# Optimization experiments

Hardware: AMD Instinct MI355X
Metric: run time of the kernel (lower is better)

## Reference

```python
import jax, jax.numpy as jnp
import numpy as np

N, K, C, L = 8192, 12, 128, 6
FF = 4 * C
SIG_LO, SIG_HI = 1.0, 5.0
BOX = 25.0

TRI_NAMES = ("ln_g", "ln_b", "Wa", "ba", "Wga", "bga", "Wb", "bb", "Wgb", "bgb",
             "lno_g", "lno_b", "Wo", "bo", "Wgo", "bgo")
FFN_NAMES = ("ln_g", "ln_b", "W1", "b1", "W2", "b2")


def _ln(x, g, b, eps=1e-5):
    m = jnp.mean(x, axis=-1, keepdims=True)
    v = jnp.mean((x - m) ** 2, axis=-1, keepdims=True)
    return (x - m) * jax.lax.rsqrt(v + eps) * g + b


def _knn_embed(coords):
    # pairwise distances -> k smallest (self included), Gaussian RBF bank over C sigmas
    d2 = jnp.sum((coords[:, None, :] - coords[None, :, :]) ** 2, axis=-1)  # [N,N]
    dist = jnp.sqrt(jnp.maximum(d2, 0.0))
    neg_d, nbr = jax.lax.top_k(-dist, K)                      # [N,K]
    k_dist = -neg_d
    sig = jnp.linspace(SIG_LO, SIG_HI, C)                     # [C]
    g = jnp.exp(-(k_dist[..., None] ** 2) / (2.0 * sig ** 2))  # [N,K,C]
    vals = jnp.where(g > 0.1, g, 0.0)                         # threshold as in repo
    vals = jnp.where(jnp.isnan(vals), 0.0, vals)
    return nbr, vals


def _transpose_vals(v, nbr):
    # sparse rowcol_transpose: value of edge (j,i) aligned to slot of edge (i,j); 0 if absent
    n = nbr.shape[0]
    nn = nbr[nbr]                                   # [N,K,K]: neighbor lists of each neighbor j
    eq = nn == jnp.arange(n)[:, None, None]         # slot where j lists i back
    pos = jnp.argmax(eq, axis=-1)                   # [N,K]
    found = jnp.any(eq, axis=-1)                    # [N,K]
    tv = v[nbr, pos]                                # [N,K,C] value at edge (j,i)
    return jnp.where(found[..., None], tv, jnp.zeros_like(tv))


def _tri_update(v, nbr, p, incoming):
    x = _ln(v, p["ln_g"], p["ln_b"])
    a = jax.nn.sigmoid(x @ p["Wga"] + p["bga"]) * (x @ p["Wa"] + p["ba"])
    b = jax.nn.sigmoid(x @ p["Wgb"] + p["bgb"]) * (x @ p["Wb"] + p["bb"])
    if incoming:  # column/incoming update operates on transposed edges
        a = _transpose_vals(a, nbr)
        b = _transpose_vals(b, nbr)
    # sparse triangle multiplicative update over KNN neighbor slots
    k = jnp.einsum('ntc,nmtc->nmc', a, b[nbr])      # [N,K,C]
    o = _ln(k, p["lno_g"], p["lno_b"]) @ p["Wo"] + p["bo"]
    return jax.nn.sigmoid(x @ p["Wgo"] + p["bgo"]) * o


def _ffn(v, p):
    x = _ln(v, p["ln_g"], p["ln_b"])
    return jax.nn.gelu(x @ p["W1"] + p["b1"], approximate=False) @ p["W2"] + p["b2"]


def _forward(coords, tri, ffn, dec_W, dec_b):
    nbr, v = _knn_embed(coords)
    v = jax.lax.stop_gradient(v)  # embedding runs under torch.no_grad in the original

    def step(v, lp):
        tp, fp = lp
        p_row = {n: t[0] for n, t in zip(TRI_NAMES, tp)}
        p_col = {n: t[1] for n, t in zip(TRI_NAMES, tp)}
        v = v + _tri_update(v, nbr, p_row, False)   # row (outgoing) update
        v = v + _tri_update(v, nbr, p_col, True)    # col (incoming) update
        v = v + _ffn(v, dict(zip(FFN_NAMES, fp)))
        return v, None

    v, _ = jax.lax.scan(jax.checkpoint(step), v, (tri, ffn))
    s = v + _transpose_vals(v, nbr)                 # sparse_operation(edge, edge^T, op='sum')
    e = s @ dec_W + dec_b                           # [N,K,1] decode
    rows = jnp.repeat(jnp.arange(N), K)
    dense = jnp.zeros((N, N, e.shape[-1]), e.dtype)
    dense = dense.at[rows, nbr.reshape(-1)].add(e.reshape(-1, e.shape[-1]))
    return dense                                    # [N,N,1] like .to_dense()


def setup_inputs() -> dict:
    key = jax.random.key(0)
    ks = jax.random.split(key, 8)
    coords = jax.random.uniform(ks[0], (N, 3), jnp.float32) * BOX

    def lin(k, fin, fout, pre=()):
        kw, _ = jax.random.split(k)
        W = jax.random.normal(kw, pre + (fin, fout), jnp.float32) / np.sqrt(fin).astype(np.float32)
        b = jnp.zeros(pre + (fout,), jnp.float32)
        return W, b

    inp = {"coords": coords}
    k_iter = iter(jax.random.split(ks[1], 16))
    pre = (L, 2)
    inp["tri_ln_g"] = jnp.ones(pre + (C,), jnp.float32)
    inp["tri_ln_b"] = jnp.zeros(pre + (C,), jnp.float32)
    for nm in ("a", "ga", "b", "gb", "o", "go"):
        W, b = lin(next(k_iter), C, C, pre)
        inp[f"tri_W{nm}"] = W
        inp[f"tri_b{nm}"] = b
    inp["tri_lno_g"] = jnp.ones(pre + (C,), jnp.float32)
    inp["tri_lno_b"] = jnp.zeros(pre + (C,), jnp.float32)
    inp["ffn_ln_g"] = jnp.ones((L, C), jnp.float32)
    inp["ffn_ln_b"] = jnp.zeros((L, C), jnp.float32)
    inp["ffn_W1"], inp["ffn_b1"] = lin(next(k_iter), C, FF, (L,))
    inp["ffn_W2"], inp["ffn_b2"] = lin(next(k_iter), FF, C, (L,))
    inp["dec_W"], inp["dec_b"] = lin(next(k_iter), C, 1)
    return inp


def reference(coords, tri_ln_g, tri_ln_b, tri_Wa, tri_ba, tri_Wga, tri_bga,
              tri_Wb, tri_bb, tri_Wgb, tri_bgb, tri_lno_g, tri_lno_b,
              tri_Wo, tri_bo, tri_Wgo, tri_bgo,
              ffn_ln_g, ffn_ln_b, ffn_W1, ffn_b1, ffn_W2, ffn_b2,
              dec_W, dec_b):
    tri = (tri_ln_g, tri_ln_b, tri_Wa, tri_ba, tri_Wga, tri_bga,
           tri_Wb, tri_bb, tri_Wgb, tri_bgb, tri_lno_g, tri_lno_b,
           tri_Wo, tri_bo, tri_Wgo, tri_bgo)
    ffn = (ffn_ln_g, ffn_ln_b, ffn_W1, ffn_b1, ffn_W2, ffn_b2)
    return _forward(coords, tri, ffn, dec_W, dec_b)
```

## Files before the change

### kernel.cpp

```cpp
#include <hip/hip_runtime.h>
#include <hip/hip_bf16.h>
#include <stdint.h>
#include <stddef.h>

#define NPTS 8192
#define KNN  12
#define CH   128
#define FFD  512
#define MEDGE (NPTS * KNN)

typedef __attribute__((ext_vector_type(8))) _Float16 half8;
typedef __attribute__((ext_vector_type(4))) _Float16 half4;
typedef __attribute__((ext_vector_type(4))) float f32x4;

__device__ __forceinline__ float wave_sum(float v) {
#pragma unroll
  for (int off = 32; off > 0; off >>= 1) v += __shfl_xor(v, off, 64);
  return v;
}
__device__ __forceinline__ float sigm_(float x) { return 1.0f / (1.0f + expf(-x)); }
__device__ __forceinline__ float gelu_(float x) { return 0.5f * x * (1.0f + erff(x * 0.7071067811865475f)); }

__global__ __launch_bounds__(256)
void prep_coords(const float* __restrict__ c, float4* __restrict__ c4)
{
  int i = blockIdx.x * 256 + threadIdx.x;
  if (i < NPTS) c4[i] = make_float4(c[3 * i], c[3 * i + 1], c[3 * i + 2], 0.0f);
}

struct SwzArgs {
  const float* src[8];
  _Float16* dst[8];
  int K[8], N[8], B[8], perB[8];
};

__global__ __launch_bounds__(256)
void prep_weights_swz(SwzArgs sa)
{
  int g = blockIdx.y;
  int idx = blockIdx.x * 256 + threadIdx.x;
  int perB = sa.perB[g];
  if (idx >= sa.B[g] * perB) return;
  int K = sa.K[g], N = sa.N[g];
  int b = idx / perB;
  int c = idx - b * perB;
  int l16 = c & 15;
  int quad = (c >> 4) & 3;
  int rest = c >> 6;
  int kts = K >> 5;
  int kt = rest % kts;
  int mt = rest / kts;
  const float* sp = sa.src[g] + ((size_t)b * K + kt * 32 + quad * 8) * N + mt * 16 + l16;
  _Float16* dp = sa.dst[g] + ((size_t)b * perB + c) * 8;
#pragma unroll
  for (int e = 0; e < 8; ++e) dp[e] = (_Float16)sp[(size_t)e * N];
}

#define KNN_CAP 2048

__global__ __launch_bounds__(256)
void knn_embed(const float4* __restrict__ coords4, const float* __restrict__ lng,
               const float* __restrict__ lnb, int* __restrict__ nbr,
               float* __restrict__ v0, _Float16* __restrict__ xln)
{
#pragma clang fp contract(off)
  __shared__ unsigned long long buf[KNN_CAP];
  __shared__ unsigned long long sel[KNN];
  __shared__ int cnt_s;
  const int i = blockIdx.x;
  const int tid = threadIdx.x;
  const int lane = tid & 63;
  const int wv = tid >> 6;
  const float4 ci = coords4[i];

  float T2 = 9.0f;
  int cnt;
  while (true) {
    if (tid == 0) cnt_s = 0;
    __syncthreads();
    for (int j = tid; j < NPTS; j += 256) {
      float4 cj = coords4[j];
      float dx = ci.x - cj.x;
      float dy = ci.y - cj.y;
      float dz = ci.z - cj.z;
      float d2 = dx * dx + dy * dy + dz * dz;
      if (d2 < T2) {
        unsigned long long key =
            (((unsigned long long)__float_as_uint(sqrtf(d2))) << 32) | (unsigned int)j;
        int idx = atomicAdd(&cnt_s, 1);
        if (idx < KNN_CAP) buf[idx] = key;
      }
    }
    __syncthreads();
    cnt = cnt_s;
    if (cnt >= KNN) break;
    T2 *= 4.0f;
    __syncthreads();
  }
  if (cnt > KNN_CAP) cnt = KNN_CAP;

  if (wv == 0) {
    unsigned long long best[KNN];
#pragma unroll
    for (int q = 0; q < KNN; ++q) best[q] = ~0ULL;
    for (int p2 = lane; p2 < cnt; p2 += 64) {
      unsigned long long key = buf[p2];
      if (key < best[KNN - 1]) {
        best[KNN - 1] = key;
#pragma unroll
        for (int q = KNN - 2; q >= 0; --q) {
          if (best[q + 1] < best[q]) { unsigned long long t = best[q]; best[q] = best[q + 1]; best[q + 1] = t; }
        }
      }
    }
    int p = 0;
    for (int r = 0; r < KNN; ++r) {
      unsigned long long c = ~0ULL;
#pragma unroll
      for (int q = 0; q < KNN; ++q) if (q == p) c = best[q];
      unsigned long long m = c;
#pragma unroll
      for (int off = 32; off > 0; off >>= 1) {
        unsigned long long o = __shfl_xor(m, off, 64);
        if (o < m) m = o;
      }
      if (c == m) ++p;
      if (lane == 0) sel[r] = m;
    }
  }
  __syncthreads();
  if (tid < KNN) nbr[i * KNN + tid] = (int)(unsigned int)(sel[tid] & 0xFFFFFFFFULL);

  float g1 = lng[lane], g2 = lng[lane + 64];
  float bb1 = lnb[lane], bb2 = lnb[lane + 64];
  for (int k = wv * 3; k < wv * 3 + 3; ++k) {
    float d = __uint_as_float((unsigned int)(sel[k] >> 32));
    float sig1 = (float)(1.0 + 4.0 * (double)lane / 127.0);
    float sig2 = (float)(1.0 + 4.0 * (double)(lane + 64) / 127.0);
    float e1 = expf((-(d * d)) / (2.0f * sig1 * sig1));
    float e2 = expf((-(d * d)) / (2.0f * sig2 * sig2));
    float v1 = (e1 > 0.1f) ? e1 : 0.0f;
    float v2 = (e2 > 0.1f) ? e2 : 0.0f;
    size_t off = (size_t)(i * KNN + k) * CH;
    v0[off + lane] = v1;
    v0[off + lane + 64] = v2;
    float m = wave_sum(v1 + v2) * (1.0f / 128.0f);
    float d1 = v1 - m, d2 = v2 - m;
    float var = wave_sum(d1 * d1 + d2 * d2) * (1.0f / 128.0f);
    float rs = 1.0f / sqrtf(var + 1e-5f);
    xln[off + lane]      = (_Float16)(d1 * rs * g1 + bb1);
    xln[off + lane + 64] = (_Float16)(d2 * rs * g2 + bb2);
  }
}

__global__ __launch_bounds__(256)
void build_tidx(const int* __restrict__ nbr, int* __restrict__ tidx)
{
  int e = blockIdx.x * 256 + threadIdx.x;
  if (e >= MEDGE) return;
  int i = e / KNN;
  int j = nbr[e];
  int res = -1;
#pragma unroll
  for (int t = 0; t < KNN; ++t) {
    if (nbr[j * KNN + t] == i) { res = j * KNN + t; break; }
  }
  tidx[e] = res;
}

__global__ __launch_bounds__(256)
void gemm_ab_go(const _Float16* __restrict__ xln,
                const _Float16* __restrict__ wa,  const float* __restrict__ ba,
                const _Float16* __restrict__ wga, const float* __restrict__ bga,
                const _Float16* __restrict__ wb,  const float* __restrict__ bb,
                const _Float16* __restrict__ wgb, const float* __restrict__ bgb,
                const _Float16* __restrict__ wgo, const float* __restrict__ bgo,
                _Float16* __restrict__ aout, _Float16* __restrict__ bout,
                _Float16* __restrict__ gobout)
{
  const int lane = threadIdx.x & 63;
  const int quad = lane >> 4;
  const int l16 = lane & 15;
  const int gw = blockIdx.x * 4 + (threadIdx.x >> 6);
  const int base = gw * 32;
  const int chbase = quad * 16 + l16;

  half8 xf[2][4];
#pragma unroll
  for (int rt = 0; rt < 2; ++rt)
#pragma unroll
    for (int kt = 0; kt < 4; ++kt)
      xf[rt][kt] = *(const half8*)(xln + (size_t)(base + rt * 16 + l16) * CH + kt * 32 + quad * 8);

  const half8* WA  = (const half8*)wa;
  const half8* WGA = (const half8*)wga;
  const half8* WB  = (const half8*)wb;
  const half8* WGB = (const half8*)wgb;
  const half8* WGO = (const half8*)wgo;

#pragma unroll
  for (int mt = 0; mt < 8; ++mt) {
    f32x4 aA[2], aGA[2], aB[2], aGB[2], aGO[2];
    const f32x4 z = {0.f, 0.f, 0.f, 0.f};
#pragma unroll
    for (int rt = 0; rt < 2; ++rt) { aA[rt] = z; aGA[rt] = z; aB[rt] = z; aGB[rt] = z; aGO[rt] = z; }
#pragma unroll
    for (int kt = 0; kt < 4; ++kt) {
      int ch = (mt * 4 + kt) * 64 + chbase;
      half8 wfa = WA[ch], wfga = WGA[ch], wfb = WB[ch], wfgb = WGB[ch], wfgo = WGO[ch];
#pragma unroll
      for (int rt = 0; rt < 2; ++rt) {
        aA[rt]  = __builtin_amdgcn_mfma_f32_16x16x32_f16(wfa,  xf[rt][kt], aA[rt], 0, 0, 0);
        aGA[rt] = __builtin_amdgcn_mfma_f32_16x16x32_f16(wfga, xf[rt][kt], aGA[rt], 0, 0, 0);
        aB[rt]  = __builtin_amdgcn_mfma_f32_16x16x32_f16(wfb,  xf[rt][kt], aB[rt], 0, 0, 0);
        aGB[rt] = __builtin_amdgcn_mfma_f32_16x16x32_f16(wfgb, xf[rt][kt], aGB[rt], 0, 0, 0);
        aGO[rt] = __builtin_amdgcn_mfma_f32_16x16x32_f16(wfgo, xf[rt][kt], aGO[rt], 0, 0, 0);
      }
    }
    f32x4 bva  = *(const f32x4*)(ba  + mt * 16 + quad * 4);
    f32x4 bvga = *(const f32x4*)(bga + mt * 16 + quad * 4);
    f32x4 bvb  = *(const f32x4*)(bb  + mt * 16 + quad * 4);
    f32x4 bvgb = *(const f32x4*)(bgb + mt * 16 + quad * 4);
    f32x4 bvgo = *(const f32x4*)(bgo + mt * 16 + quad * 4);
#pragma unroll
    for (int rt = 0; rt < 2; ++rt) {
      half4 av, bv, gv;
#pragma unroll
      for (int r = 0; r < 4; ++r) {
        av[r] = (_Float16)(sigm_(aGA[rt][r] + bvga[r]) * (aA[rt][r] + bva[r]));
        bv[r] = (_Float16)(sigm_(aGB[rt][r] + bvgb[r]) * (aB[rt][r] + bvb[r]));
        gv[r] = (_Float16)(sigm_(aGO[rt][r] + bvgo[r]));
      }
      size_t off = (size_t)(base + rt * 16 + l16) * CH + mt * 16 + quad * 4;
      *(half4*)(aout + off) = av;
      *(half4*)(bout + off) = bv;
      *(half4*)(gobout + off) = gv;
    }
  }
}

__global__ __launch_bounds__(192)
void tri_og(const _Float16* __restrict__ a, const _Float16* __restrict__ b,
            const int* __restrict__ nbr, const int* __restrict__ tidx,
            const float* __restrict__ lng, const float* __restrict__ lnb,
            const _Float16* __restrict__ wo, const float* __restrict__ bo,
            const _Float16* __restrict__ gob, float* __restrict__ v,
            const float* __restrict__ nlng, const float* __restrict__ nlnb,
            _Float16* __restrict__ xlnN, int incoming)
{
  __shared__ alignas(16) _Float16 As[48][136];
  __shared__ alignas(16) _Float16 klds[48][136];
  __shared__ int bidx[4][KNN][KNN];
  __shared__ int nbr_s[4][KNN];
  const int n0 = blockIdx.x * 4;
  const int tid = threadIdx.x;

  if (tid < 48) nbr_s[tid / KNN][tid % KNN] = nbr[n0 * KNN + tid];
  __syncthreads();
  for (int it = tid; it < 4 * KNN * KNN; it += 192) {
    int nn = it / (KNN * KNN);
    int r = it - nn * KNN * KNN;
    int m = r / KNN, t = r - m * KNN;
    int j = nbr_s[nn][m];
    bidx[nn][m][t] = incoming ? tidx[j * KNN + t] : (j * KNN + t);
  }
  for (int it = tid; it < 4 * KNN * 16; it += 192) {
    int nn = it / (KNN * 16);
    int r = it - nn * (KNN * 16);
    int t = r >> 4;
    int c8 = (r & 15) * 8;
    half8 av;
    if (incoming) {
      int ti = tidx[(size_t)(n0 + nn) * KNN + t];
      if (ti >= 0) av = *(const half8*)(a + (size_t)ti * CH + c8);
      else {
#pragma unroll
        for (int e = 0; e < 8; ++e) av[e] = (_Float16)0.0f;
      }
    } else {
      av = *(const half8*)(a + (size_t)((n0 + nn) * KNN + t) * CH + c8);
    }
    *(half8*)&As[nn * KNN + t][c8] = av;
  }
  __syncthreads();

  const int m2 = tid >> 4;
  const int c8 = (tid & 15) * 8;
  for (int nn = 0; nn < 4; ++nn) {
    float acc[8];
#pragma unroll
    for (int r = 0; r < 8; ++r) acc[r] = 0.0f;
#pragma unroll
    for (int t = 0; t < KNN; ++t) {
      int bi = bidx[nn][m2][t];
      if (bi >= 0) {
        half8 bv = *(const half8*)(b + (size_t)bi * CH + c8);
        half8 av = *(const half8*)&As[nn * KNN + t][c8];
#pragma unroll
        for (int r = 0; r < 8; ++r) acc[r] += (float)av[r] * (float)bv[r];
      }
    }
    float s = 0.0f, sq = 0.0f;
#pragma unroll
    for (int r = 0; r < 8; ++r) { s += acc[r]; sq += acc[r] * acc[r]; }
#pragma unroll
    for (int off = 1; off < 16; off <<= 1) {
      s += __shfl_xor(s, off, 64);
      sq += __shfl_xor(sq, off, 64);
    }
    float mean = s * (1.0f / 128.0f);
    float var = sq * (1.0f / 128.0f) - mean * mean;
    if (var < 0.0f) var = 0.0f;
    float rs = 1.0f / sqrtf(var + 1e-5f);
    half8 o;
#pragma unroll
    for (int r = 0; r < 8; ++r)
      o[r] = (_Float16)((acc[r] - mean) * rs * lng[c8 + r] + lnb[c8 + r]);
    *(half8*)&klds[nn * KNN + m2][c8] = o;
  }
  __syncthreads();

  const int lane = tid & 63;
  const int w = tid >> 6;
  const int quad = lane >> 4;
  const int l16 = lane & 15;
  const int chbase = quad * 16 + l16;
  const size_t rowOff = (size_t)(blockIdx.x * 48 + w * 16 + l16) * CH;

  half8 kf[4];
#pragma unroll
  for (int kt = 0; kt < 4; ++kt)
    kf[kt] = *(const half8*)&klds[w * 16 + l16][kt * 32 + quad * 8];

  const half8* WO = (const half8*)wo;
  f32x4 vn[8];
  float s = 0.0f, sq = 0.0f;
#pragma unroll
  for (int mt = 0; mt < 8; ++mt) {
    f32x4 acc = {0.f, 0.f, 0.f, 0.f};
#pragma unroll
    for (int kt = 0; kt < 4; ++kt)
      acc = __builtin_amdgcn_mfma_f32_16x16x32_f16(WO[(mt * 4 + kt) * 64 + chbase], kf[kt], acc, 0, 0, 0);
    half4 g4 = *(const half4*)(gob + rowOff + mt * 16 + quad * 4);
    f32x4 bo4 = *(const f32x4*)(bo + mt * 16 + quad * 4);
    f32x4 vv = *(const f32x4*)(v + rowOff + mt * 16 + quad * 4);
#pragma unroll
    for (int r = 0; r < 4; ++r) {
      float nv = vv[r] + (float)g4[r] * (acc[r] + bo4[r]);
      vn[mt][r] = nv;
      s += nv;
      sq += nv * nv;
    }
    *(f32x4*)(v + rowOff + mt * 16 + quad * 4) = vn[mt];
  }
  s  += __shfl_xor(s, 16, 64);  s  += __shfl_xor(s, 32, 64);
  sq += __shfl_xor(sq, 16, 64); sq += __shfl_xor(sq, 32, 64);
  float mean = s * (1.0f / 128.0f);
  float var = sq * (1.0f / 128.0f) - mean * mean;
  if (var < 0.0f) var = 0.0f;
  float rs = 1.0f / sqrtf(var + 1e-5f);
#pragma unroll
  for (int mt = 0; mt < 8; ++mt) {
    f32x4 g4 = *(const f32x4*)(nlng + mt * 16 + quad * 4);
    f32x4 b4 = *(const f32x4*)(nlnb + mt * 16 + quad * 4);
    half4 o;
#pragma unroll
    for (int r = 0; r < 4; ++r)
      o[r] = (_Float16)((vn[mt][r] - mean) * rs * g4[r] + b4[r]);
    *(half4*)(xlnN + rowOff + mt * 16 + quad * 4) = o;
  }
}

#define HADDR(row, ch) ((((row) * 64 + ((ch) ^ ((row) & 7)))) * 8)

__global__ __launch_bounds__(256)
void ffn_fused(const _Float16* __restrict__ xln,
               const _Float16* __restrict__ w1, const float* __restrict__ b1,
               const _Float16* __restrict__ w2, const float* __restrict__ b2,
               float* __restrict__ v,
               const float* __restrict__ nlng, const float* __restrict__ nlnb,
               _Float16* __restrict__ xlnN)
{
  __shared__ alignas(16) _Float16 hlds[32 * FFD];
  __shared__ float part[32][4][2];
  const int tid = threadIdx.x;
  const int lane = tid & 63;
  const int w = tid >> 6;
  const int quad = lane >> 4;
  const int l16 = lane & 15;
  const int rowBase = blockIdx.x * 32;
  const int chbase = quad * 16 + l16;

  half8 xf[2][4];
#pragma unroll
  for (int rt = 0; rt < 2; ++rt)
#pragma unroll
    for (int kt = 0; kt < 4; ++kt)
      xf[rt][kt] = *(const half8*)(xln + (size_t)(rowBase + rt * 16 + l16) * CH + kt * 32 + quad * 8);

  const half8* W1 = (const half8*)w1;
#pragma unroll
  for (int mt = 0; mt < 8; ++mt) {
    int mtg = w * 8 + mt;
    f32x4 acc[2];
    const f32x4 z = {0.f, 0.f, 0.f, 0.f};
    acc[0] = z; acc[1] = z;
#pragma unroll
    for (int kt = 0; kt < 4; ++kt) {
      half8 wf = W1[(mtg * 4 + kt) * 64 + chbase];
#pragma unroll
      for (int rt = 0; rt < 2; ++rt)
        acc[rt] = __builtin_amdgcn_mfma_f32_16x16x32_f16(wf, xf[rt][kt], acc[rt], 0, 0, 0);
    }
    f32x4 bv = *(const f32x4*)(b1 + mtg * 16 + quad * 4);
    int ch = mtg * 2 + (quad >> 1);
    int sub = (quad & 1) * 4;
#pragma unroll
    for (int rt = 0; rt < 2; ++rt) {
      int row = rt * 16 + l16;
      half4 hh;
#pragma unroll
      for (int r = 0; r < 4; ++r)
        hh[r] = (_Float16)(gelu_(acc[rt][r] + bv[r]));
      *(half4*)&hlds[HADDR(row, ch) + sub] = hh;
    }
  }
  __syncthreads();

  const half8* W2 = (const half8*)w2;
  f32x4 vn2[2][2];
  float s2[2] = {0.f, 0.f}, q2[2] = {0.f, 0.f};
#pragma unroll
  for (int m2 = 0; m2 < 2; ++m2) {
    int mt = w * 2 + m2;
    f32x4 accA[2], accB[2];
    const f32x4 z = {0.f, 0.f, 0.f, 0.f};
    accA[0] = z; accA[1] = z; accB[0] = z; accB[1] = z;
#pragma unroll
    for (int kt = 0; kt < 16; kt += 2) {
      half8 wf0 = W2[(mt * 16 + kt) * 64 + chbase];
      half8 wf1 = W2[(mt * 16 + kt + 1) * 64 + chbase];
#pragma unroll
      for (int rt = 0; rt < 2; ++rt) {
        int row = rt * 16 + l16;
        half8 hf0 = *(const half8*)&hlds[HADDR(row, kt * 4 + quad)];
        half8 hf1 = *(const half8*)&hlds[HADDR(row, (kt + 1) * 4 + quad)];
        accA[rt] = __builtin_amdgcn_mfma_f32_16x16x32_f16(wf0, hf0, accA[rt], 0, 0, 0);
        accB[rt] = __builtin_amdgcn_mfma_f32_16x16x32_f16(wf1, hf1, accB[rt], 0, 0, 0);
      }
    }
    f32x4 bv = *(const f32x4*)(b2 + mt * 16 + quad * 4);
#pragma unroll
    for (int rt = 0; rt < 2; ++rt) {
      size_t off = (size_t)(rowBase + rt * 16 + l16) * CH + mt * 16 + quad * 4;
      f32x4 vv = *(const f32x4*)(v + off);
#pragma unroll
      for (int r = 0; r < 4; ++r) {
        float nv = vv[r] + accA[rt][r] + accB[rt][r] + bv[r];
        vn2[m2][rt][r] = nv;
        s2[rt] += nv;
        q2[rt] += nv * nv;
      }
      *(f32x4*)(v + off) = vn2[m2][rt];
    }
  }
#pragma unroll
  for (int rt = 0; rt < 2; ++rt) {
    float ss = s2[rt], qq = q2[rt];
    ss += __shfl_xor(ss, 16, 64); ss += __shfl_xor(ss, 32, 64);
    qq += __shfl_xor(qq, 16, 64); qq += __shfl_xor(qq, 32, 64);
    if (quad == 0) { part[rt * 16 + l16][w][0] = ss; part[rt * 16 + l16][w][1] = qq; }
  }
  __syncthreads();
#pragma unroll
  for (int rt = 0; rt < 2; ++rt) {
    int row = rt * 16 + l16;
    float su = part[row][0][0] + part[row][1][0] + part[row][2][0] + part[row][3][0];
    float qu = part[row][0][1] + part[row][1][1] + part[row][2][1] + part[row][3][1];
    float mean = su * (1.0f / 128.0f);
    float var = qu * (1.0f / 128.0f) - mean * mean;
    if (var < 0.0f) var = 0.0f;
    float rs = 1.0f / sqrtf(var + 1e-5f);
#pragma unroll
    for (int m2 = 0; m2 < 2; ++m2) {
      int mt = w * 2 + m2;
      f32x4 g4 = *(const f32x4*)(nlng + mt * 16 + quad * 4);
      f32x4 b4 = *(const f32x4*)(nlnb + mt * 16 + quad * 4);
      half4 o;
#pragma unroll
      for (int r = 0; r < 4; ++r)
        o[r] = (_Float16)((vn2[m2][rt][r] - mean) * rs * g4[r] + b4[r]);
      *(half4*)(xlnN + (size_t)(rowBase + row) * CH + mt * 16 + quad * 4) = o;
    }
  }
}

__global__ __launch_bounds__(256)
void decode_row(const float* __restrict__ vin, const int* __restrict__ tidx,
                const int* __restrict__ nbr, const float* __restrict__ decW,
                const float* __restrict__ decB, float* __restrict__ out)
{
  __shared__ float ev[KNN];
  __shared__ int nbr_s[KNN];
  const int n = blockIdx.x;
  const int tid = threadIdx.x;
  const int lane = tid & 63;
  const int w = tid >> 6;
  if (tid < KNN) nbr_s[tid] = nbr[n * KNN + tid];
  float dw1 = decW[lane], dw2 = decW[lane + 64];
  for (int k = w; k < KNN; k += 4) {
    int e = n * KNN + k;
    int ti = tidx[e];
    float s1 = vin[(size_t)e * CH + lane];
    float s2 = vin[(size_t)e * CH + 64 + lane];
    if (ti >= 0) {
      s1 += vin[(size_t)ti * CH + lane];
      s2 += vin[(size_t)ti * CH + 64 + lane];
    }
    float tot = wave_sum(s1 * dw1 + s2 * dw2);
    if (lane == 0) ev[k] = tot + decB[0];
  }
  __syncthreads();
  float4 z = make_float4(0.f, 0.f, 0.f, 0.f);
  float4* row = (float4*)(out + (size_t)n * NPTS);
  for (int idx = tid; idx < NPTS / 4; idx += 256) row[idx] = z;
  __syncthreads();
  if (tid < KNN) out[(size_t)n * NPTS + nbr_s[tid]] = ev[tid];
}

extern "C" void kernel_launch(void* const* d_in, const int* in_sizes, int n_in,
                              void* d_out, int out_size, void* d_ws, size_t ws_size,
                              hipStream_t stream)
{
  (void)in_sizes; (void)n_in; (void)out_size; (void)ws_size;
  const float* coords  = (const float*)d_in[0];
  const float* t_ln_g  = (const float*)d_in[1];
  const float* t_ln_b  = (const float*)d_in[2];
  const float* t_Wa    = (const float*)d_in[3];
  const float* t_ba    = (const float*)d_in[4];
  const float* t_Wga   = (const float*)d_in[5];
  const float* t_bga   = (const float*)d_in[6];
  const float* t_Wb    = (const float*)d_in[7];
  const float* t_bb    = (const float*)d_in[8];
  const float* t_Wgb   = (const float*)d_in[9];
  const float* t_bgb   = (const float*)d_in[10];
  const float* t_Wo    = (const float*)d_in[11];
  const float* t_bo    = (const float*)d_in[12];
  const float* t_Wgo   = (const float*)d_in[13];
  const float* t_bgo   = (const float*)d_in[14];
  const float* t_lno_g = (const float*)d_in[15];
  const float* t_lno_b = (const float*)d_in[16];
  const float* f_ln_g  = (const float*)d_in[17];
  const float* f_ln_b  = (const float*)d_in[18];
  const float* f_W1    = (const float*)d_in[19];
  const float* f_b1    = (const float*)d_in[20];
  const float* f_W2    = (const float*)d_in[21];
  const float* f_b2    = (const float*)d_in[22];
  const float* dec_W   = (const float*)d_in[23];
  const float* dec_b   = (const float*)d_in[24];

  const size_t NKC = (size_t)MEDGE * CH;
  char* ws = (char*)d_ws;
  float* v        = (float*)(ws);
  _Float16* gx    = (_Float16*)(ws + NKC * 6);
  int* nbr        = (int*)(ws + NKC * 8);
  int* tidx       = (int*)(ws + NKC * 8 + (size_t)MEDGE * 4);
  float4* coords4 = (float4*)(ws + NKC * 8 + (size_t)MEDGE * 8);
  _Float16* wbase = (_Float16*)(ws + NKC * 8 + (size_t)MEDGE * 8 + NPTS * 16);
  const size_t TRIH = (size_t)12 * 2048 * 8;
  _Float16* wA  = wbase;
  _Float16* wGA = wA  + TRIH;
  _Float16* wB  = wGA + TRIH;
  _Float16* wGB = wB  + TRIH;
  _Float16* wGO = wGB + TRIH;
  _Float16* wO  = wGO + TRIH;
  _Float16* w1  = wO  + TRIH;
  _Float16* w2  = w1  + (size_t)6 * 8192 * 8;

  _Float16* abuf = (_Float16*)d_out;
  _Float16* bbuf = abuf + NKC;

  prep_coords<<<32, 256, 0, stream>>>(coords, coords4);

  SwzArgs sa;
  sa.src[0] = t_Wa;  sa.dst[0] = wA;  sa.K[0] = CH;  sa.N[0] = CH;  sa.B[0] = 12; sa.perB[0] = 2048;
  sa.src[1] = t_Wga; sa.dst[1] = wGA; sa.K[1] = CH;  sa.N[1] = CH;  sa.B[1] = 12; sa.perB[1] = 2048;
  sa.src[2] = t_Wb;  sa.dst[2] = wB;  sa.K[2] = CH;  sa.N[2] = CH;  sa.B[2] = 12; sa.perB[2] = 2048;
  sa.src[3] = t_Wgb; sa.dst[3] = wGB; sa.K[3] = CH;  sa.N[3] = CH;  sa.B[3] = 12; sa.perB[3] = 2048;
  sa.src[4] = t_Wgo; sa.dst[4] = wGO; sa.K[4] = CH;  sa.N[4] = CH;  sa.B[4] = 12; sa.perB[4] = 2048;
  sa.src[5] = t_Wo;  sa.dst[5] = wO;  sa.K[5] = CH;  sa.N[5] = CH;  sa.B[5] = 12; sa.perB[5] = 2048;
  sa.src[6] = f_W1;  sa.dst[6] = w1;  sa.K[6] = CH;  sa.N[6] = FFD; sa.B[6] = 6;  sa.perB[6] = 8192;
  sa.src[7] = f_W2;  sa.dst[7] = w2;  sa.K[7] = FFD; sa.N[7] = CH;  sa.B[7] = 6;  sa.perB[7] = 8192;
  dim3 pgrid(192, 8);
  prep_weights_swz<<<pgrid, 256, 0, stream>>>(sa);

  knn_embed<<<NPTS, 256, 0, stream>>>(coords4, t_ln_g, t_ln_b, nbr, v, gx);
  build_tidx<<<MEDGE / 256, 256, 0, stream>>>(nbr, tidx);

  const size_t WS = (size_t)2048 * 8;
  gemm_ab_go<<<MEDGE / 128, 256, 0, stream>>>(gx,
      wA, t_ba, wGA, t_bga, wB, t_bb, wGB, t_bgb, wGO, t_bgo,
      abuf, bbuf, gx);

  for (int l = 0; l < 6; ++l) {
    int s0 = 2 * l, s1 = 2 * l + 1, s2 = 2 * l + 2;
    tri_og<<<NPTS / 4, 192, 0, stream>>>(abuf, bbuf, nbr, tidx,
        t_lno_g + s0 * CH, t_lno_b + s0 * CH,
        wO + s0 * WS, t_bo + s0 * CH, gx, v,
        t_ln_g + s1 * CH, t_ln_b + s1 * CH, gx, 0);
    gemm_ab_go<<<MEDGE / 128, 256, 0, stream>>>(gx,
        wA + s1 * WS, t_ba + s1 * CH, wGA + s1 * WS, t_bga + s1 * CH,
        wB + s1 * WS, t_bb + s1 * CH, wGB + s1 * WS, t_bgb + s1 * CH,
        wGO + s1 * WS, t_bgo + s1 * CH,
        abuf, bbuf, gx);
    tri_og<<<NPTS / 4, 192, 0, stream>>>(abuf, bbuf, nbr, tidx,
        t_lno_g + s1 * CH, t_lno_b + s1 * CH,
        wO + s1 * WS, t_bo + s1 * CH, gx, v,
        f_ln_g + l * CH, f_ln_b + l * CH, gx, 1);
    const float* ng = (l < 5) ? (t_ln_g + s2 * CH) : t_ln_g;
    const float* nb = (l < 5) ? (t_ln_b + s2 * CH) : t_ln_b;
    ffn_fused<<<MEDGE / 32, 256, 0, stream>>>(gx,
        w1 + (size_t)l * 8192 * 8, f_b1 + l * FFD,
        w2 + (size_t)l * 8192 * 8, f_b2 + l * CH,
        v, ng, nb, gx);
    if (l < 5) {
      gemm_ab_go<<<MEDGE / 128, 256, 0, stream>>>(gx,
          wA + s2 * WS, t_ba + s2 * CH, wGA + s2 * WS, t_bga + s2 * CH,
          wB + s2 * WS, t_bb + s2 * CH, wGB + s2 * WS, t_bgb + s2 * CH,
          wGO + s2 * WS, t_bgo + s2 * CH,
          abuf, bbuf, gx);
    }
  }

  decode_row<<<NPTS, 256, 0, stream>>>(v, tidx, nbr, dec_W, dec_b, (float*)d_out);
}
```

Measured before the change: 2.563 ms.

## Fuse next-stage gated projection GEMMs into triangle and FFN epilogues

```diff
diff --git a/kernel.cpp b/kernel.cpp
--- a/kernel.cpp
+++ b/kernel.cpp
@@ -20,6 +20,8 @@
 }
 __device__ __forceinline__ float sigm_(float x) { return 1.0f / (1.0f + expf(-x)); }
 __device__ __forceinline__ float gelu_(float x) { return 0.5f * x * (1.0f + erff(x * 0.7071067811865475f)); }
+
+#define XADDR(row, ch) ((((row) * 16 + ((ch) ^ ((row) & 7)))) * 8)
 
 __global__ __launch_bounds__(256)
 void prep_coords(const float* __restrict__ c, float4* __restrict__ c4)
@@ -240,13 +242,19 @@
 }
 
 __global__ __launch_bounds__(192)
-void tri_og(const _Float16* __restrict__ a, const _Float16* __restrict__ b,
-            const int* __restrict__ nbr, const int* __restrict__ tidx,
-            const float* __restrict__ lng, const float* __restrict__ lnb,
-            const _Float16* __restrict__ wo, const float* __restrict__ bo,
-            const _Float16* __restrict__ gob, float* __restrict__ v,
-            const float* __restrict__ nlng, const float* __restrict__ nlnb,
-            _Float16* __restrict__ xlnN, int incoming)
+void tri_og_ab(const _Float16* __restrict__ a, const _Float16* __restrict__ b,
+               const int* __restrict__ nbr, const int* __restrict__ tidx,
+               const float* __restrict__ lng, const float* __restrict__ lnb,
+               const _Float16* __restrict__ wo, const float* __restrict__ bo,
+               const _Float16* __restrict__ gob, float* __restrict__ v,
+               const float* __restrict__ nlng, const float* __restrict__ nlnb,
+               const _Float16* __restrict__ wa,  const float* __restrict__ ba,
+               const _Float16* __restrict__ wga, const float* __restrict__ bga,
+               const _Float16* __restrict__ wb,  const float* __restrict__ bb,
+               const _Float16* __restrict__ wgb, const float* __restrict__ bgb,
+               const _Float16* __restrict__ wgo2, const float* __restrict__ bgo2,
+               _Float16* __restrict__ aout, _Float16* __restrict__ bout,
+               _Float16* __restrict__ gobout, int incoming)
 {
   __shared__ alignas(16) _Float16 As[48][136];
   __shared__ alignas(16) _Float16 klds[48][136];
@@ -325,12 +333,14 @@
   const int quad = lane >> 4;
   const int l16 = lane & 15;
   const int chbase = quad * 16 + l16;
-  const size_t rowOff = (size_t)(blockIdx.x * 48 + w * 16 + l16) * CH;
+  const int rowL = w * 16 + l16;
+  const size_t rowOff = (size_t)(blockIdx.x * 48 + rowL) * CH;
+  _Float16* xsw = &As[0][0];
 
   half8 kf[4];
 #pragma unroll
   for (int kt = 0; kt < 4; ++kt)
-    kf[kt] = *(const half8*)&klds[w * 16 + l16][kt * 32 + quad * 8];
+    kf[kt] = *(const half8*)&klds[rowL][kt * 32 + quad * 8];
 
   const half8* WO = (const half8*)wo;
   f32x4 vn[8];
@@ -367,6 +377,178 @@
 #pragma unroll
     for (int r = 0; r < 4; ++r)
       o[r] = (_Float16)((vn[mt][r] - mean) * rs * g4[r] + b4[r]);
+    int ch = mt * 2 + (quad >> 1);
+    *(half4*)&xsw[XADDR(rowL, ch) + (quad & 1) * 4] = o;
+  }
+  half8 xf[4];
+#pragma unroll
+  for (int kt = 0; kt < 4; ++kt)
+    xf[kt] = *(const half8*)&xsw[XADDR(rowL, kt * 4 + quad)];
+
+  const half8* WA  = (const half8*)wa;
+  const half8* WGA = (const half8*)wga;
+  const half8* WB  = (const half8*)wb;
+  const half8* WGB = (const half8*)wgb;
+  const half8* WGO = (const half8*)wgo2;
+#pragma unroll
+  for (int mt = 0; mt < 8; ++mt) {
+    f32x4 aA = {0.f,0.f,0.f,0.f}, aGA = aA, aB = aA, aGB = aA, aGO = aA;
+#pragma unroll
+    for (int kt = 0; kt < 4; ++kt) {
+      int ch = (mt * 4 + kt) * 64 + chbase;
+      aA  = __builtin_amdgcn_mfma_f32_16x16x32_f16(WA[ch],  xf[kt], aA, 0, 0, 0);
+      aGA = __builtin_amdgcn_mfma_f32_16x16x32_f16(WGA[ch], xf[kt], aGA, 0, 0, 0);
+      aB  = __builtin_amdgcn_mfma_f32_16x16x32_f16(WB[ch],  xf[kt], aB, 0, 0, 0);
+      aGB = __builtin_amdgcn_mfma_f32_16x16x32_f16(WGB[ch], xf[kt], aGB, 0, 0, 0);
+      aGO = __builtin_amdgcn_mfma_f32_16x16x32_f16(WGO[ch], xf[kt], aGO, 0, 0, 0);
+    }
+    f32x4 bva  = *(const f32x4*)(ba   + mt * 16 + quad * 4);
+    f32x4 bvga = *(const f32x4*)(bga  + mt * 16 + quad * 4);
+    f32x4 bvb  = *(const f32x4*)(bb   + mt * 16 + quad * 4);
+    f32x4 bvgb = *(const f32x4*)(bgb  + mt * 16 + quad * 4);
+    f32x4 bvgo = *(const f32x4*)(bgo2 + mt * 16 + quad * 4);
+    half4 av, bv, gv;
+#pragma unroll
+    for (int r = 0; r < 4; ++r) {
+      av[r] = (_Float16)(sigm_(aGA[r] + bvga[r]) * (aA[r] + bva[r]));
+      bv[r] = (_Float16)(sigm_(aGB[r] + bvgb[r]) * (aB[r] + bvb[r]));
+      gv[r] = (_Float16)(sigm_(aGO[r] + bvgo[r]));
+    }
+    size_t off = rowOff + mt * 16 + quad * 4;
+    *(half4*)(aout + off) = av;
+    *(half4*)(bout + off) = bv;
+    *(half4*)(gobout + off) = gv;
+  }
+}
+
+__global__ __launch_bounds__(192)
+void tri_og(const _Float16* __restrict__ a, const _Float16* __restrict__ b,
+            const int* __restrict__ nbr, const int* __restrict__ tidx,
+            const float* __restrict__ lng, const float* __restrict__ lnb,
+            const _Float16* __restrict__ wo, const float* __restrict__ bo,
+            const _Float16* __restrict__ gob, float* __restrict__ v,
+            const float* __restrict__ nlng, const float* __restrict__ nlnb,
+            _Float16* __restrict__ xlnN, int incoming)
+{
+  __shared__ alignas(16) _Float16 As[48][136];
+  __shared__ alignas(16) _Float16 klds[48][136];
+  __shared__ int bidx[4][KNN][KNN];
+  __shared__ int nbr_s[4][KNN];
+  const int n0 = blockIdx.x * 4;
+  const int tid = threadIdx.x;
+
+  if (tid < 48) nbr_s[tid / KNN][tid % KNN] = nbr[n0 * KNN + tid];
+  __syncthreads();
+  for (int it = tid; it < 4 * KNN * KNN; it += 192) {
+    int nn = it / (KNN * KNN);
+    int r = it - nn * KNN * KNN;
+    int m = r / KNN, t = r - m * KNN;
+    int j = nbr_s[nn][m];
+    bidx[nn][m][t] = incoming ? tidx[j * KNN + t] : (j * KNN + t);
+  }
+  for (int it = tid; it < 4 * KNN * 16; it += 192) {
+    int nn = it / (KNN * 16);
+    int r = it - nn * (KNN * 16);
+    int t = r >> 4;
+    int c8 = (r & 15) * 8;
+    half8 av;
+    if (incoming) {
+      int ti = tidx[(size_t)(n0 + nn) * KNN + t];
+      if (ti >= 0) av = *(const half8*)(a + (size_t)ti * CH + c8);
+      else {
+#pragma unroll
+        for (int e = 0; e < 8; ++e) av[e] = (_Float16)0.0f;
+      }
+    } else {
+      av = *(const half8*)(a + (size_t)((n0 + nn) * KNN + t) * CH + c8);
+    }
+    *(half8*)&As[nn * KNN + t][c8] = av;
+  }
+  __syncthreads();
+
+  const int m2 = tid >> 4;
+  const int c8 = (tid & 15) * 8;
+  for (int nn = 0; nn < 4; ++nn) {
+    float acc[8];
+#pragma unroll
+    for (int r = 0; r < 8; ++r) acc[r] = 0.0f;
+#pragma unroll
+    for (int t = 0; t < KNN; ++t) {
+      int bi = bidx[nn][m2][t];
+      if (bi >= 0) {
+        half8 bv = *(const half8*)(b + (size_t)bi * CH + c8);
+        half8 av = *(const half8*)&As[nn * KNN + t][c8];
+#pragma unroll
+        for (int r = 0; r < 8; ++r) acc[r] += (float)av[r] * (float)bv[r];
+      }
+    }
+    float s = 0.0f, sq = 0.0f;
+#pragma unroll
+    for (int r = 0; r < 8; ++r) { s += acc[r]; sq += acc[r] * acc[r]; }
+#pragma unroll
+    for (int off = 1; off < 16; off <<= 1) {
+      s += __shfl_xor(s, off, 64);
+      sq += __shfl_xor(sq, off, 64);
+    }
+    float mean = s * (1.0f / 128.0f);
+    float var = sq * (1.0f / 128.0f) - mean * mean;
+    if (var < 0.0f) var = 0.0f;
+    float rs = 1.0f / sqrtf(var + 1e-5f);
+    half8 o;
+#pragma unroll
+    for (int r = 0; r < 8; ++r)
+      o[r] = (_Float16)((acc[r] - mean) * rs * lng[c8 + r] + lnb[c8 + r]);
+    *(half8*)&klds[nn * KNN + m2][c8] = o;
+  }
+  __syncthreads();
+
+  const int lane = tid & 63;
+  const int w = tid >> 6;
+  const int quad = lane >> 4;
+  const int l16 = lane & 15;
+  const int chbase = quad * 16 + l16;
+  const size_t rowOff = (size_t)(blockIdx.x * 48 + w * 16 + l16) * CH;
+
+  half8 kf[4];
+#pragma unroll
+  for (int kt = 0; kt < 4; ++kt)
+    kf[kt] = *(const half8*)&klds[w * 16 + l16][kt * 32 + quad * 8];
+
+  const half8* WO = (const half8*)wo;
+  f32x4 vn[8];
+  float s = 0.0f, sq = 0.0f;
+#pragma unroll
+  for (int mt = 0; mt < 8; ++mt) {
+    f32x4 acc = {0.f, 0.f, 0.f, 0.f};
+#pragma unroll
+    for (int kt = 0; kt < 4; ++kt)
+      acc = __builtin_amdgcn_mfma_f32_16x16x32_f16(WO[(mt * 4 + kt) * 64 + chbase], kf[kt], acc, 0, 0, 0);
+    half4 g4 = *(const half4*)(gob + rowOff + mt * 16 + quad * 4);
+    f32x4 bo4 = *(const f32x4*)(bo + mt * 16 + quad * 4);
+    f32x4 vv = *(const f32x4*)(v + rowOff + mt * 16 + quad * 4);
+#pragma unroll
+    for (int r = 0; r < 4; ++r) {
+      float nv = vv[r] + (float)g4[r] * (acc[r] + bo4[r]);
+      vn[mt][r] = nv;
+      s += nv;
+      sq += nv * nv;
+    }
+    *(f32x4*)(v + rowOff + mt * 16 + quad * 4) = vn[mt];
+  }
+  s  += __shfl_xor(s, 16, 64);  s  += __shfl_xor(s, 32, 64);
+  sq += __shfl_xor(sq, 16, 64); sq += __shfl_xor(sq, 32, 64);
+  float mean = s * (1.0f / 128.0f);
+  float var = sq * (1.0f / 128.0f) - mean * mean;
+  if (var < 0.0f) var = 0.0f;
+  float rs = 1.0f / sqrtf(var + 1e-5f);
+#pragma unroll
+  for (int mt = 0; mt < 8; ++mt) {
+    f32x4 g4 = *(const f32x4*)(nlng + mt * 16 + quad * 4);
+    f32x4 b4 = *(const f32x4*)(nlnb + mt * 16 + quad * 4);
+    half4 o;
+#pragma unroll
+    for (int r = 0; r < 4; ++r)
+      o[r] = (_Float16)((vn[mt][r] - mean) * rs * g4[r] + b4[r]);
     *(half4*)(xlnN + rowOff + mt * 16 + quad * 4) = o;
   }
 }
@@ -374,12 +556,18 @@
 #define HADDR(row, ch) ((((row) * 64 + ((ch) ^ ((row) & 7)))) * 8)
 
 __global__ __launch_bounds__(256)
-void ffn_fused(const _Float16* __restrict__ xln,
-               const _Float16* __restrict__ w1, const float* __restrict__ b1,
-               const _Float16* __restrict__ w2, const float* __restrict__ b2,
-               float* __restrict__ v,
-               const float* __restrict__ nlng, const float* __restrict__ nlnb,
-               _Float16* __restrict__ xlnN)
+void ffn_ab(const _Float16* __restrict__ xln,
+            const _Float16* __restrict__ w1, const float* __restrict__ b1,
+            const _Float16* __restrict__ w2, const float* __restrict__ b2,
+            float* __restrict__ v,
+            const float* __restrict__ nlng, const float* __restrict__ nlnb,
+            const _Float16* __restrict__ wa,  const float* __restrict__ ba,
+            const _Float16* __restrict__ wga, const float* __restrict__ bga,
+            const _Float16* __restrict__ wb,  const float* __restrict__ bb,
+            const _Float16* __restrict__ wgb, const float* __restrict__ bgb,
+            const _Float16* __restrict__ wgo2, const float* __restrict__ bgo2,
+            _Float16* __restrict__ aout, _Float16* __restrict__ bout,
+            _Float16* __restrict__ gobout, int doAB)
 {
   __shared__ alignas(16) _Float16 hlds[32 * FFD];
   __shared__ float part[32][4][2];
@@ -464,6 +652,8 @@
       *(f32x4*)(v + off) = vn2[m2][rt];
     }
   }
+  if (!doAB) return;
+
 #pragma unroll
   for (int rt = 0; rt < 2; ++rt) {
     float ss = s2[rt], qq = q2[rt];
@@ -472,6 +662,8 @@
     if (quad == 0) { part[rt * 16 + l16][w][0] = ss; part[rt * 16 + l16][w][1] = qq; }
   }
   __syncthreads();
+
+  _Float16* xsw = hlds;
 #pragma unroll
   for (int rt = 0; rt < 2; ++rt) {
     int row = rt * 16 + l16;
@@ -490,7 +682,62 @@
 #pragma unroll
       for (int r = 0; r < 4; ++r)
         o[r] = (_Float16)((vn2[m2][rt][r] - mean) * rs * g4[r] + b4[r]);
-      *(half4*)(xlnN + (size_t)(rowBase + row) * CH + mt * 16 + quad * 4) = o;
+      int ch = mt * 2 + (quad >> 1);
+      *(half4*)&xsw[XADDR(row, ch) + (quad & 1) * 4] = o;
+    }
+  }
+  __syncthreads();
+
+  half8 xfD[2][4];
+#pragma unroll
+  for (int rt = 0; rt < 2; ++rt)
+#pragma unroll
+    for (int kt = 0; kt < 4; ++kt)
+      xfD[rt][kt] = *(const half8*)&xsw[XADDR(rt * 16 + l16, kt * 4 + quad)];
+
+  const half8* WA  = (const half8*)wa;
+  const half8* WGA = (const half8*)wga;
+  const half8* WB  = (const half8*)wb;
+  const half8* WGB = (const half8*)wgb;
+  const half8* WGO = (const half8*)wgo2;
+#pragma unroll
+  for (int m2 = 0; m2 < 2; ++m2) {
+    int mt = w * 2 + m2;
+    f32x4 aA[2], aGA[2], aB[2], aGB[2], aGO[2];
+    const f32x4 z = {0.f, 0.f, 0.f, 0.f};
+#pragma unroll
+    for (int rt = 0; rt < 2; ++rt) { aA[rt] = z; aGA[rt] = z; aB[rt] = z; aGB[rt] = z; aGO[rt] = z; }
+#pragma unroll
+    for (int kt = 0; kt < 4; ++kt) {
+      int ch = (mt * 4 + kt) * 64 + chbase;
+      half8 wfa = WA[ch], wfga = WGA[ch], wfb = WB[ch], wfgb = WGB[ch], wfgo = WGO[ch];
+#pragma unroll
+      for (int rt = 0; rt < 2; ++rt) {
+        aA[rt]  = __builtin_amdgcn_mfma_f32_16x16x32_f16(wfa,  xfD[rt][kt], aA[rt], 0, 0, 0);
+        aGA[rt] = __builtin_amdgcn_mfma_f32_16x16x32_f16(wfga, xfD[rt][kt], aGA[rt], 0, 0, 0);
+        aB[rt]  = __builtin_amdgcn_mfma_f32_16x16x32_f16(wfb,  xfD[rt][kt], aB[rt], 0, 0, 0);
+        aGB[rt] = __builtin_amdgcn_mfma_f32_16x16x32_f16(wfgb, xfD[rt][kt], aGB[rt], 0, 0, 0);
+        aGO[rt] = __builtin_amdgcn_mfma_f32_16x16x32_f16(wfgo, xfD[rt][kt], aGO[rt], 0, 0, 0);
+      }
+    }
+    f32x4 bva  = *(const f32x4*)(ba   + mt * 16 + quad * 4);
+    f32x4 bvga = *(const f32x4*)(bga  + mt * 16 + quad * 4);
+    f32x4 bvb  = *(const f32x4*)(bb   + mt * 16 + quad * 4);
+    f32x4 bvgb = *(const f32x4*)(bgb  + mt * 16 + quad * 4);
+    f32x4 bvgo = *(const f32x4*)(bgo2 + mt * 16 + quad * 4);
+#pragma unroll
+    for (int rt = 0; rt < 2; ++rt) {
+      half4 av, bv, gv;
+#pragma unroll
+      for (int r = 0; r < 4; ++r) {
+        av[r] = (_Float16)(sigm_(aGA[rt][r] + bvga[r]) * (aA[rt][r] + bva[r]));
+        bv[r] = (_Float16)(sigm_(aGB[rt][r] + bvgb[r]) * (aB[rt][r] + bvb[r]));
+        gv[r] = (_Float16)(sigm_(aGO[rt][r] + bvgo[r]));
+      }
+      size_t off = (size_t)(rowBase + rt * 16 + l16) * CH + mt * 16 + quad * 4;
+      *(half4*)(aout + off) = av;
+      *(half4*)(bout + off) = bv;
+      *(half4*)(gobout + off) = gv;
     }
   }
 }
@@ -577,8 +824,10 @@
   _Float16* w1  = wO  + TRIH;
   _Float16* w2  = w1  + (size_t)6 * 8192 * 8;
 
-  _Float16* abuf = (_Float16*)d_out;
-  _Float16* bbuf = abuf + NKC;
+  _Float16* a0 = (_Float16*)d_out;
+  _Float16* b0 = a0 + NKC;
+  _Float16* a1 = b0 + NKC;
+  _Float16* b1 = a1 + NKC;
 
   prep_coords<<<32, 256, 0, stream>>>(coords, coords4);
 
@@ -600,36 +849,32 @@
   const size_t WS = (size_t)2048 * 8;
   gemm_ab_go<<<MEDGE / 128, 256, 0, stream>>>(gx,
       wA, t_ba, wGA, t_bga, wB, t_bb, wGB, t_bgb, wGO, t_bgo,
-      abuf, bbuf, gx);
+      a0, b0, gx);
 
   for (int l = 0; l < 6; ++l) {
     int s0 = 2 * l, s1 = 2 * l + 1, s2 = 2 * l + 2;
-    tri_og<<<NPTS / 4, 192, 0, stream>>>(abuf, bbuf, nbr, tidx,
+    tri_og_ab<<<NPTS / 4, 192, 0, stream>>>(a0, b0, nbr, tidx,
         t_lno_g + s0 * CH, t_lno_b + s0 * CH,
         wO + s0 * WS, t_bo + s0 * CH, gx, v,
-        t_ln_g + s1 * CH, t_ln_b + s1 * CH, gx, 0);
-    gemm_ab_go<<<MEDGE / 128, 256, 0, stream>>>(gx,
+        t_ln_g + s1 * CH, t_ln_b + s1 * CH,
         wA + s1 * WS, t_ba + s1 * CH, wGA + s1 * WS, t_bga + s1 * CH,
         wB + s1 * WS, t_bb + s1 * CH, wGB + s1 * WS, t_bgb + s1 * CH,
         wGO + s1 * WS, t_bgo + s1 * CH,
-        abuf, bbuf, gx);
-    tri_og<<<NPTS / 4, 192, 0, stream>>>(abuf, bbuf, nbr, tidx,
+        a1, b1, gx, 0);
+    tri_og<<<NPTS / 4, 192, 0, stream>>>(a1, b1, nbr, tidx,
         t_lno_g + s1 * CH, t_lno_b + s1 * CH,
         wO + s1 * WS, t_bo + s1 * CH, gx, v,
         f_ln_g + l * CH, f_ln_b + l * CH, gx, 1);
-    const float* ng = (l < 5) ? (t_ln_g + s2 * CH) : t_ln_g;
-    const float* nb = (l < 5) ? (t_ln_b + s2 * CH) : t_ln_b;
-    ffn_fused<<<MEDGE / 32, 256, 0, stream>>>(gx,
+    int doAB = (l < 5) ? 1 : 0;
+    int sw = doAB ? s2 : 0;
+    ffn_ab<<<MEDGE / 32, 256, 0, stream>>>(gx,
         w1 + (size_t)l * 8192 * 8, f_b1 + l * FFD,
         w2 + (size_t)l * 8192 * 8, f_b2 + l * CH,
-        v, ng, nb, gx);
-    if (l < 5) {
-      gemm_ab_go<<<MEDGE / 128, 256, 0, stream>>>(gx,
-          wA + s2 * WS, t_ba + s2 * CH, wGA + s2 * WS, t_bga + s2 * CH,
-          wB + s2 * WS, t_bb + s2 * CH, wGB + s2 * WS, t_bgb + s2 * CH,
-          wGO + s2 * WS, t_bgo + s2 * CH,
-          abuf, bbuf, gx);
-    }
+        v, t_ln_g + sw * CH, t_ln_b + sw * CH,
+        wA + sw * WS, t_ba + sw * CH, wGA + sw * WS, t_bga + sw * CH,
+        wB + sw * WS, t_bb + sw * CH, wGB + sw * WS, t_bgb + sw * CH,
+        wGO + sw * WS, t_bgo + sw * CH,
+        a0, b0, gx, doAB);
   }
 
   decode_row<<<NPTS, 256, 0, stream>>>(v, tidx, nbr, dec_W, dec_b, (float*)d_out);
```

Result: slower. 3.270 ms (+27.6%).

## Reorder points by Morton cell for gather locality and swizzle tri_og blocks

Applied to the files above, without the earlier changes.

```diff
diff --git a/kernel.cpp b/kernel.cpp
--- a/kernel.cpp
+++ b/kernel.cpp
@@ -8,6 +8,7 @@
 #define CH   128
 #define FFD  512
 #define MEDGE (NPTS * KNN)
+#define NCELL 512
 
 typedef __attribute__((ext_vector_type(8))) _Float16 half8;
 typedef __attribute__((ext_vector_type(4))) _Float16 half4;
@@ -21,11 +22,64 @@
 __device__ __forceinline__ float sigm_(float x) { return 1.0f / (1.0f + expf(-x)); }
 __device__ __forceinline__ float gelu_(float x) { return 0.5f * x * (1.0f + erff(x * 0.7071067811865475f)); }
 
+#define HADDR(row, ch) ((((row) * 64 + ((ch) ^ ((row) & 7)))) * 8)
+
+__device__ __forceinline__ int morton3(int x, int y, int z) {
+  int m = 0;
+#pragma unroll
+  for (int b = 0; b < 3; ++b)
+    m |= (((x >> b) & 1) << (3 * b + 2)) | (((y >> b) & 1) << (3 * b + 1)) | (((z >> b) & 1) << (3 * b));
+  return m;
+}
+
+__global__ __launch_bounds__(512)
+void zero_hist(int* __restrict__ hist)
+{
+  hist[threadIdx.x] = 0;
+}
+
 __global__ __launch_bounds__(256)
-void prep_coords(const float* __restrict__ c, float4* __restrict__ c4)
+void prep_coords(const float* __restrict__ c, float4* __restrict__ c4,
+                 int* __restrict__ cell, int* __restrict__ hist)
 {
   int i = blockIdx.x * 256 + threadIdx.x;
-  if (i < NPTS) c4[i] = make_float4(c[3 * i], c[3 * i + 1], c[3 * i + 2], 0.0f);
+  if (i >= NPTS) return;
+  float x = c[3 * i], y = c[3 * i + 1], z = c[3 * i + 2];
+  c4[i] = make_float4(x, y, z, 0.0f);
+  int cx = (int)(x * (8.0f / 25.0f)); if (cx > 7) cx = 7; if (cx < 0) cx = 0;
+  int cy = (int)(y * (8.0f / 25.0f)); if (cy > 7) cy = 7; if (cy < 0) cy = 0;
+  int cz = (int)(z * (8.0f / 25.0f)); if (cz > 7) cz = 7; if (cz < 0) cz = 0;
+  int cl = morton3(cx, cy, cz);
+  cell[i] = cl;
+  atomicAdd(&hist[cl], 1);
+}
+
+__global__ __launch_bounds__(512)
+void prefix512(const int* __restrict__ hist, int* __restrict__ base)
+{
+  __shared__ int tmp[NCELL];
+  int t = threadIdx.x;
+  tmp[t] = hist[t];
+  __syncthreads();
+  for (int off = 1; off < NCELL; off <<= 1) {
+    int v = tmp[t];
+    if (t >= off) v += tmp[t - off];
+    __syncthreads();
+    tmp[t] = v;
+    __syncthreads();
+  }
+  base[t] = tmp[t] - hist[t];
+}
+
+__global__ __launch_bounds__(256)
+void scatter_perm(const int* __restrict__ cell, int* __restrict__ base,
+                  int* __restrict__ rank, int* __restrict__ perm)
+{
+  int i = blockIdx.x * 256 + threadIdx.x;
+  if (i >= NPTS) return;
+  int r = atomicAdd(&base[cell[i]], 1);
+  rank[i] = r;
+  perm[r] = i;
 }
 
 struct SwzArgs {
@@ -59,9 +113,10 @@
 #define KNN_CAP 2048
 
 __global__ __launch_bounds__(256)
-void knn_embed(const float4* __restrict__ coords4, const float* __restrict__ lng,
-               const float* __restrict__ lnb, int* __restrict__ nbr,
-               float* __restrict__ v0, _Float16* __restrict__ xln)
+void knn_embed(const float4* __restrict__ coords4, const int* __restrict__ perm,
+               const int* __restrict__ rank,
+               const float* __restrict__ lng, const float* __restrict__ lnb,
+               int* __restrict__ nbr, float* __restrict__ v0, _Float16* __restrict__ xln)
 {
 #pragma clang fp contract(off)
   __shared__ unsigned long long buf[KNN_CAP];
@@ -71,7 +126,7 @@
   const int tid = threadIdx.x;
   const int lane = tid & 63;
   const int wv = tid >> 6;
-  const float4 ci = coords4[i];
+  const float4 ci = coords4[perm[i]];
 
   float T2 = 9.0f;
   int cnt;
@@ -129,7 +184,8 @@
     }
   }
   __syncthreads();
-  if (tid < KNN) nbr[i * KNN + tid] = (int)(unsigned int)(sel[tid] & 0xFFFFFFFFULL);
+  if (tid < KNN)
+    nbr[i * KNN + tid] = rank[(int)(unsigned int)(sel[tid] & 0xFFFFFFFFULL)];
 
   float g1 = lng[lane], g2 = lng[lane + 64];
   float bb1 = lnb[lane], bb2 = lnb[lane + 64];
@@ -252,7 +308,8 @@
   __shared__ alignas(16) _Float16 klds[48][136];
   __shared__ int bidx[4][KNN][KNN];
   __shared__ int nbr_s[4][KNN];
-  const int n0 = blockIdx.x * 4;
+  const int blk = blockIdx.x;
+  const int n0 = ((blk & 7) * 256 + (blk >> 3)) * 4;
   const int tid = threadIdx.x;
 
   if (tid < 48) nbr_s[tid / KNN][tid % KNN] = nbr[n0 * KNN + tid];
@@ -325,7 +382,7 @@
   const int quad = lane >> 4;
   const int l16 = lane & 15;
   const int chbase = quad * 16 + l16;
-  const size_t rowOff = (size_t)(blockIdx.x * 48 + w * 16 + l16) * CH;
+  const size_t rowOff = (size_t)(n0 * KNN + w * 16 + l16) * CH;
 
   half8 kf[4];
 #pragma unroll
@@ -370,8 +427,6 @@
     *(half4*)(xlnN + rowOff + mt * 16 + quad * 4) = o;
   }
 }
-
-#define HADDR(row, ch) ((((row) * 64 + ((ch) ^ ((row) & 7)))) * 8)
 
 __global__ __launch_bounds__(256)
 void ffn_fused(const _Float16* __restrict__ xln,
@@ -497,16 +552,17 @@
 
 __global__ __launch_bounds__(256)
 void decode_row(const float* __restrict__ vin, const int* __restrict__ tidx,
-                const int* __restrict__ nbr, const float* __restrict__ decW,
-                const float* __restrict__ decB, float* __restrict__ out)
+                const int* __restrict__ nbr, const int* __restrict__ perm,
+                const float* __restrict__ decW, const float* __restrict__ decB,
+                float* __restrict__ out)
 {
   __shared__ float ev[KNN];
-  __shared__ int nbr_s[KNN];
+  __shared__ int col_s[KNN];
   const int n = blockIdx.x;
   const int tid = threadIdx.x;
   const int lane = tid & 63;
   const int w = tid >> 6;
-  if (tid < KNN) nbr_s[tid] = nbr[n * KNN + tid];
+  if (tid < KNN) col_s[tid] = perm[nbr[n * KNN + tid]];
   float dw1 = decW[lane], dw2 = decW[lane + 64];
   for (int k = w; k < KNN; k += 4) {
     int e = n * KNN + k;
@@ -521,11 +577,12 @@
     if (lane == 0) ev[k] = tot + decB[0];
   }
   __syncthreads();
+  const int orig_n = perm[n];
   float4 z = make_float4(0.f, 0.f, 0.f, 0.f);
-  float4* row = (float4*)(out + (size_t)n * NPTS);
+  float4* row = (float4*)(out + (size_t)orig_n * NPTS);
   for (int idx = tid; idx < NPTS / 4; idx += 256) row[idx] = z;
   __syncthreads();
-  if (tid < KNN) out[(size_t)n * NPTS + nbr_s[tid]] = ev[tid];
+  if (tid < KNN) out[(size_t)orig_n * NPTS + col_s[tid]] = ev[tid];
 }
 
 extern "C" void kernel_launch(void* const* d_in, const int* in_sizes, int n_in,
@@ -565,8 +622,14 @@
   _Float16* gx    = (_Float16*)(ws + NKC * 6);
   int* nbr        = (int*)(ws + NKC * 8);
   int* tidx       = (int*)(ws + NKC * 8 + (size_t)MEDGE * 4);
-  float4* coords4 = (float4*)(ws + NKC * 8 + (size_t)MEDGE * 8);
-  _Float16* wbase = (_Float16*)(ws + NKC * 8 + (size_t)MEDGE * 8 + NPTS * 16);
+  char* aux       = ws + NKC * 8 + (size_t)MEDGE * 8;
+  float4* coords4 = (float4*)(aux);
+  int* cell       = (int*)(aux + NPTS * 16);
+  int* hist       = (int*)(aux + NPTS * 16 + NPTS * 4);
+  int* base       = (int*)(aux + NPTS * 16 + NPTS * 4 + NCELL * 4);
+  int* rank       = (int*)(aux + NPTS * 16 + NPTS * 4 + NCELL * 8);
+  int* perm       = (int*)(aux + NPTS * 16 + NPTS * 8 + NCELL * 8);
+  _Float16* wbase = (_Float16*)(aux + NPTS * 16 + NPTS * 12 + NCELL * 8);
   const size_t TRIH = (size_t)12 * 2048 * 8;
   _Float16* wA  = wbase;
   _Float16* wGA = wA  + TRIH;
@@ -580,7 +643,10 @@
   _Float16* abuf = (_Float16*)d_out;
   _Float16* bbuf = abuf + NKC;
 
-  prep_coords<<<32, 256, 0, stream>>>(coords, coords4);
+  zero_hist<<<1, 512, 0, stream>>>(hist);
+  prep_coords<<<32, 256, 0, stream>>>(coords, coords4, cell, hist);
+  prefix512<<<1, 512, 0, stream>>>(hist, base);
+  scatter_perm<<<32, 256, 0, stream>>>(cell, base, rank, perm);
 
   SwzArgs sa;
   sa.src[0] = t_Wa;  sa.dst[0] = wA;  sa.K[0] = CH;  sa.N[0] = CH;  sa.B[0] = 12; sa.perB[0] = 2048;
@@ -594,7 +660,7 @@
   dim3 pgrid(192, 8);
   prep_weights_swz<<<pgrid, 256, 0, stream>>>(sa);
 
-  knn_embed<<<NPTS, 256, 0, stream>>>(coords4, t_ln_g, t_ln_b, nbr, v, gx);
+  knn_embed<<<NPTS, 256, 0, stream>>>(coords4, perm, rank, t_ln_g, t_ln_b, nbr, v, gx);
   build_tidx<<<MEDGE / 256, 256, 0, stream>>>(nbr, tidx);
 
   const size_t WS = (size_t)2048 * 8;
@@ -632,5 +698,5 @@
     }
   }
 
-  decode_row<<<NPTS, 256, 0, stream>>>(v, tidx, nbr, dec_W, dec_b, (float*)d_out);
-}
+  decode_row<<<NPTS, 256, 0, stream>>>(v, tidx, nbr, perm, dec_W, dec_b, (float*)d_out);
+}
```

Measured after the change: 2.435 ms (median of 2 runs). 1.05x faster.
